# Kernel tuning notes

Hardware: AMD Instinct MI355X
Metric: run time of the kernel (lower is better)

Reference implementation:

```python
import jax, jax.numpy as jnp
import numpy as np

IN_F, OUT_F = 4096, 11008
B, S = 4, 512

def setup_inputs() -> dict:
    key = jax.random.key(0)
    k1, k2, k3, k4 = jax.random.split(key, 4)
    x = jax.random.normal(k1, (B, S, IN_F), dtype=jnp.float16)
    # int8 quantized weights in [-127, 127]
    weight_q = jax.random.randint(k2, (OUT_F, IN_F), -127, 128, dtype=jnp.int32).astype(jnp.int8)
    # per-output-channel scale, small positive values typical of int8 quant
    scale = (jax.random.uniform(k3, (OUT_F, 1), dtype=jnp.float32) * 0.02 + 0.001).astype(jnp.float16)
    bias = (jax.random.normal(k4, (OUT_F,), dtype=jnp.float32) * 0.02).astype(jnp.float16)
    return {"x": x, "weight_q": weight_q, "scale": scale, "bias": bias}

def reference(x, weight_q, scale, bias):
    # weight_deq = weight_q.to(fp16) * scale  -> [out, in] fp16 (materialized, as in torch)
    weight_deq = weight_q.astype(scale.dtype) * scale
    # F.linear: y = x @ W^T + b
    out = jnp.einsum('bsi,oi->bso', x, weight_deq) + bias
    return out
```

## Files before the change

kernel.cpp:

```cpp
#include <hip/hip_runtime.h>
#include <stdint.h>


#define M_DIM 2048
#define N_DIM 11008
#define K_DIM 4096
#define BM 128
#define BN 128
#define BK 32
#define NKT (K_DIM / BK)

#define NWQ (N_DIM * K_DIM / 4)
#define NXQ (M_DIM * K_DIM / 4)

typedef _Float16 f16x4 __attribute__((ext_vector_type(4)));
typedef _Float16 f16x8 __attribute__((ext_vector_type(8)));
typedef float    f32x4 __attribute__((ext_vector_type(4)));

__global__ __launch_bounds__(256)
void prep_w(const int* __restrict__ WQ, const float* __restrict__ SC,
            _Float16* __restrict__ W16)
{
  const int i = blockIdx.x * 256 + threadIdx.x;
  const int4 w = ((const int4*)WQ)[i];
  const float s = SC[i >> 10];
  f16x4 o = { (_Float16)(w.x * s), (_Float16)(w.y * s),
              (_Float16)(w.z * s), (_Float16)(w.w * s) };
  ((f16x4*)W16)[i] = o;
}

__global__ __launch_bounds__(256)
void prep_x(const float* __restrict__ X, _Float16* __restrict__ X16)
{
  const int i = blockIdx.x * 256 + threadIdx.x;
  const float4 v = ((const float4*)X)[i];
  f16x4 o = { (_Float16)v.x, (_Float16)v.y, (_Float16)v.z, (_Float16)v.w };
  ((f16x4*)X16)[i] = o;
}

__device__ __forceinline__ void async_cp16(void* lds, const void* g) {
  auto l = (__attribute__((address_space(3))) uint32_t*)(uintptr_t)lds;
  auto p = (const __attribute__((address_space(1))) uint32_t*)(uintptr_t)g;
  __builtin_amdgcn_global_load_lds(p, l, 16, 0, 0);
}

__global__ __launch_bounds__(256, 5)
void qlinear_gemm(const _Float16* __restrict__ A, const _Float16* __restrict__ B,
                  const float* __restrict__ BI, float* __restrict__ O)
{
  __shared__ __align__(16) _Float16 sA[2][BM * BK];
  __shared__ __align__(16) _Float16 sB[2][BN * BK];

  const int t    = threadIdx.x;
  const int lane = t & 63;
  const int wv   = t >> 6;
  const int wr   = wv >> 1;
  const int wc   = wv & 1;
  const int fr   = lane & 15;
  const int fq   = lane >> 4;

  const int wg = (blockIdx.x & 7) * 172 + (blockIdx.x >> 3);
  const int m0 = (wg & 15) * BM;
  const int n0 = (wg >> 4) * BN;

  const _Float16* gA0 = A + (size_t)(m0 + (t >> 2)) * K_DIM + (t & 3) * 8;
  const _Float16* gB0 = B + (size_t)(n0 + (t >> 2)) * K_DIM + (t & 3) * 8;
  const int wbase = t & 0xC0;
  _Float16* lA = &sA[0][0] + wbase * 8;
  _Float16* lB = &sB[0][0] + wbase * 8;

  f32x4 acc[4][4] = {};

#define STAGE(buf, kt) do {                                                    \
    const int ko_ = (kt) * BK;                                                 \
    async_cp16((void*)(lA + (buf) * (BM * BK)),        gA0 + ko_);             \
    async_cp16((void*)(lA + (buf) * (BM * BK) + 2048), gA0 + (size_t)64 * K_DIM + ko_); \
    async_cp16((void*)(lB + (buf) * (BN * BK)),        gB0 + ko_);             \
    async_cp16((void*)(lB + (buf) * (BN * BK) + 2048), gB0 + (size_t)64 * K_DIM + ko_); \
  } while (0)

  STAGE(0, 0);
  __syncthreads();

  for (int kt = 0; kt < NKT; ++kt) {
    const int cur = kt & 1;
    if (kt + 1 < NKT) STAGE(cur ^ 1, kt + 1);

    const _Float16* aB = &sA[cur][0] + (wr * 64 + fr) * BK + fq * 8;
    const _Float16* bB = &sB[cur][0] + (wc * 64 + fr) * BK + fq * 8;

    f16x8 af[4], bf[4];
#pragma unroll
    for (int i = 0; i < 4; ++i) af[i] = *(const f16x8*)(aB + i * 16 * BK);
#pragma unroll
    for (int i = 0; i < 4; ++i) bf[i] = *(const f16x8*)(bB + i * 16 * BK);

#pragma unroll
    for (int mi = 0; mi < 4; ++mi)
#pragma unroll
      for (int ni = 0; ni < 4; ++ni)
        acc[mi][ni] = __builtin_amdgcn_mfma_f32_16x16x32_f16(af[mi], bf[ni], acc[mi][ni], 0, 0, 0);

    __syncthreads();
  }

  const int om = m0 + wr * 64;
  const int on = n0 + wc * 64;
#pragma unroll
  for (int ni = 0; ni < 4; ++ni) {
    const int n = on + ni * 16 + fr;
    const float b = BI[n];
#pragma unroll
    for (int mi = 0; mi < 4; ++mi) {
      const int m = om + mi * 16 + fq * 4;
#pragma unroll
      for (int j = 0; j < 4; ++j) {
        const _Float16 h = (_Float16)acc[mi][ni][j];
        const _Float16 r = (_Float16)((float)h + b);
        O[(size_t)(m + j) * N_DIM + n] = (float)r;
      }
    }
  }
#undef STAGE
}

extern "C" void kernel_launch(void* const* d_in, const int* in_sizes, int n_in,
                              void* d_out, int out_size, void* d_ws, size_t ws_size,
                              hipStream_t stream) {
  const float* x  = (const float*)d_in[0];
  const int*   wq = (const int*)d_in[1];
  const float* sc = (const float*)d_in[2];
  const float* bi = (const float*)d_in[3];
  float* out = (float*)d_out;

  _Float16* x16 = (_Float16*)d_ws;
  _Float16* w16 = (_Float16*)((char*)d_ws + (size_t)M_DIM * K_DIM * 2);
  const size_t need = (size_t)M_DIM * K_DIM * 2 + (size_t)N_DIM * K_DIM * 2;
  if (ws_size < need) return;

  prep_w<<<dim3(NWQ / 256), dim3(256), 0, stream>>>(wq, sc, w16);
  prep_x<<<dim3(NXQ / 256), dim3(256), 0, stream>>>(x, x16);

  dim3 grid((M_DIM / BM) * (N_DIM / BN));
  qlinear_gemm<<<grid, dim3(256), 0, stream>>>(x16, w16, bi, out);
}
```

Before: 525.1 us.

## Fuse int8 weight dequantization into GEMM B-tile staging

Drops the separate prep_w pass, which read the int32-stored weights and wrote a full fp16 dequantized copy. The GEMM now loads int32 weight values straight into registers, multiplies by a per-row scale held in registers, and writes fp16 into LDS. The next tile's loads are issued before the MFMAs to overlap latency, and launch bounds drop from 5 to 3 blocks per SM. The cost is more VGPR pressure and conversion ALU work inside the main loop. Each weight is also re-read as 4-byte int32 by all 16 M-tiles instead of as 2-byte fp16, which doubles GEMM B-side traffic.

```diff
diff --git a/kernel.cpp b/kernel.cpp
--- a/kernel.cpp
+++ b/kernel.cpp
@@ -10,24 +10,11 @@
 #define BK 32
 #define NKT (K_DIM / BK)
 
-#define NWQ (N_DIM * K_DIM / 4)
 #define NXQ (M_DIM * K_DIM / 4)
 
 typedef _Float16 f16x4 __attribute__((ext_vector_type(4)));
 typedef _Float16 f16x8 __attribute__((ext_vector_type(8)));
 typedef float    f32x4 __attribute__((ext_vector_type(4)));
-
-__global__ __launch_bounds__(256)
-void prep_w(const int* __restrict__ WQ, const float* __restrict__ SC,
-            _Float16* __restrict__ W16)
-{
-  const int i = blockIdx.x * 256 + threadIdx.x;
-  const int4 w = ((const int4*)WQ)[i];
-  const float s = SC[i >> 10];
-  f16x4 o = { (_Float16)(w.x * s), (_Float16)(w.y * s),
-              (_Float16)(w.z * s), (_Float16)(w.w * s) };
-  ((f16x4*)W16)[i] = o;
-}
 
 __global__ __launch_bounds__(256)
 void prep_x(const float* __restrict__ X, _Float16* __restrict__ X16)
@@ -44,18 +31,19 @@
   __builtin_amdgcn_global_load_lds(p, l, 16, 0, 0);
 }
 
-__global__ __launch_bounds__(256, 5)
-void qlinear_gemm(const _Float16* __restrict__ A, const _Float16* __restrict__ B,
-                  const float* __restrict__ BI, float* __restrict__ O)
+__global__ __launch_bounds__(256, 3)
+void qlinear_gemm(const _Float16* __restrict__ A, const int* __restrict__ WQ,
+                  const float* __restrict__ SC, const float* __restrict__ BI,
+                  float* __restrict__ O)
 {
   __shared__ __align__(16) _Float16 sA[2][BM * BK];
   __shared__ __align__(16) _Float16 sB[2][BN * BK];
 
   const int t    = threadIdx.x;
   const int lane = t & 63;
-  const int wv   = t >> 6;
-  const int wr   = wv >> 1;
-  const int wc   = wv & 1;
+  const int wid  = t >> 6;
+  const int wr   = wid >> 1;
+  const int wc   = wid & 1;
   const int fr   = lane & 15;
   const int fq   = lane >> 4;
 
@@ -64,27 +52,51 @@
   const int n0 = (wg >> 4) * BN;
 
   const _Float16* gA0 = A + (size_t)(m0 + (t >> 2)) * K_DIM + (t & 3) * 8;
-  const _Float16* gB0 = B + (size_t)(n0 + (t >> 2)) * K_DIM + (t & 3) * 8;
   const int wbase = t & 0xC0;
   _Float16* lA = &sA[0][0] + wbase * 8;
-  _Float16* lB = &sB[0][0] + wbase * 8;
+
+  const int brow = t >> 3;
+  const int bkq  = t & 7;
+  const int* gB = WQ + (size_t)(n0 + brow) * K_DIM + bkq * 4;
+  float s[4];
+#pragma unroll
+  for (int r = 0; r < 4; ++r) s[r] = SC[n0 + 32 * r + brow];
+  _Float16* lBw = &sB[0][0] + brow * BK + bkq * 4;
 
   f32x4 acc[4][4] = {};
 
-#define STAGE(buf, kt) do {                                                    \
+#define STAGE_A(buf, kt) do {                                                  \
     const int ko_ = (kt) * BK;                                                 \
     async_cp16((void*)(lA + (buf) * (BM * BK)),        gA0 + ko_);             \
     async_cp16((void*)(lA + (buf) * (BM * BK) + 2048), gA0 + (size_t)64 * K_DIM + ko_); \
-    async_cp16((void*)(lB + (buf) * (BN * BK)),        gB0 + ko_);             \
-    async_cp16((void*)(lB + (buf) * (BN * BK) + 2048), gB0 + (size_t)64 * K_DIM + ko_); \
   } while (0)
 
-  STAGE(0, 0);
+  STAGE_A(0, 0);
+  {
+    int4 w0[4];
+#pragma unroll
+    for (int r = 0; r < 4; ++r)
+      w0[r] = *(const int4*)(gB + (size_t)32 * r * K_DIM);
+#pragma unroll
+    for (int r = 0; r < 4; ++r) {
+      f16x4 o = { (_Float16)(w0[r].x * s[r]), (_Float16)(w0[r].y * s[r]),
+                  (_Float16)(w0[r].z * s[r]), (_Float16)(w0[r].w * s[r]) };
+      *(f16x4*)(lBw + r * 32 * BK) = o;
+    }
+  }
   __syncthreads();
 
   for (int kt = 0; kt < NKT; ++kt) {
     const int cur = kt & 1;
-    if (kt + 1 < NKT) STAGE(cur ^ 1, kt + 1);
+    const bool pf = (kt + 1 < NKT);
+
+    int4 wnx[4];
+    if (pf) {
+      STAGE_A(cur ^ 1, kt + 1);
+#pragma unroll
+      for (int r = 0; r < 4; ++r)
+        wnx[r] = *(const int4*)(gB + (kt + 1) * BK + (size_t)32 * r * K_DIM);
+    }
 
     const _Float16* aB = &sA[cur][0] + (wr * 64 + fr) * BK + fq * 8;
     const _Float16* bB = &sB[cur][0] + (wc * 64 + fr) * BK + fq * 8;
@@ -101,6 +113,14 @@
       for (int ni = 0; ni < 4; ++ni)
         acc[mi][ni] = __builtin_amdgcn_mfma_f32_16x16x32_f16(af[mi], bf[ni], acc[mi][ni], 0, 0, 0);
 
+    if (pf) {
+#pragma unroll
+      for (int r = 0; r < 4; ++r) {
+        f16x4 o = { (_Float16)(wnx[r].x * s[r]), (_Float16)(wnx[r].y * s[r]),
+                    (_Float16)(wnx[r].z * s[r]), (_Float16)(wnx[r].w * s[r]) };
+        *(f16x4*)(lBw + (cur ^ 1) * (BM * BK) + r * 32 * BK) = o;
+      }
+    }
     __syncthreads();
   }
 
@@ -121,7 +141,7 @@
       }
     }
   }
-#undef STAGE
+#undef STAGE_A
 }
 
 extern "C" void kernel_launch(void* const* d_in, const int* in_sizes, int n_in,
@@ -134,13 +154,10 @@
   float* out = (float*)d_out;
 
   _Float16* x16 = (_Float16*)d_ws;
-  _Float16* w16 = (_Float16*)((char*)d_ws + (size_t)M_DIM * K_DIM * 2);
-  const size_t need = (size_t)M_DIM * K_DIM * 2 + (size_t)N_DIM * K_DIM * 2;
-  if (ws_size < need) return;
+  if (ws_size < (size_t)M_DIM * K_DIM * 2) return;
 
-  prep_w<<<dim3(NWQ / 256), dim3(256), 0, stream>>>(wq, sc, w16);
   prep_x<<<dim3(NXQ / 256), dim3(256), 0, stream>>>(x, x16);
 
   dim3 grid((M_DIM / BM) * (N_DIM / BN));
-  qlinear_gemm<<<grid, dim3(256), 0, stream>>>(x16, w16, bi, out);
+  qlinear_gemm<<<grid, dim3(256), 0, stream>>>(x16, wq, sc, bi, out);
 }
```

Result: slower. 572.9 us (+9.1%).

## Use 16-wave blocks with BK=64 and a triple-buffered async LDS pipeline

Applied to the files above, without the earlier changes.

The GEMM block grows from 4 to 16 waves. Each wave now owns a 32x32 sub-tile instead of 64x64, and the K tile doubles to 64. Shared memory becomes a three-slot ring with explicit vmcnt waits and raw barriers, so global-to-LDS copies run two stages ahead of compute. MFMA phases are split by s_setprio and extra barriers. The aim is better latency hiding and fewer loop iterations, at the cost of lower register reuse per wave (more LDS reads per MFMA), more barriers, and 96KB of LDS that limits occupancy.

```diff
diff --git a/kernel.cpp b/kernel.cpp
--- a/kernel.cpp
+++ b/kernel.cpp
@@ -7,7 +7,7 @@
 #define K_DIM 4096
 #define BM 128
 #define BN 128
-#define BK 32
+#define BK 64
 #define NKT (K_DIM / BK)
 
 #define NWQ (N_DIM * K_DIM / 4)
@@ -44,18 +44,18 @@
   __builtin_amdgcn_global_load_lds(p, l, 16, 0, 0);
 }
 
-__global__ __launch_bounds__(256, 5)
+__global__ __launch_bounds__(1024, 4)
 void qlinear_gemm(const _Float16* __restrict__ A, const _Float16* __restrict__ B,
                   const float* __restrict__ BI, float* __restrict__ O)
 {
-  __shared__ __align__(16) _Float16 sA[2][BM * BK];
-  __shared__ __align__(16) _Float16 sB[2][BN * BK];
+  __shared__ __align__(16) _Float16 sA[3][BM * BK];
+  __shared__ __align__(16) _Float16 sB[3][BN * BK];
 
   const int t    = threadIdx.x;
   const int lane = t & 63;
-  const int wv   = t >> 6;
-  const int wr   = wv >> 1;
-  const int wc   = wv & 1;
+  const int wid  = t >> 6;
+  const int wr   = wid >> 2;
+  const int wc   = wid & 3;
   const int fr   = lane & 15;
   const int fq   = lane >> 4;
 
@@ -63,59 +63,85 @@
   const int m0 = (wg & 15) * BM;
   const int n0 = (wg >> 4) * BN;
 
-  const _Float16* gA0 = A + (size_t)(m0 + (t >> 2)) * K_DIM + (t & 3) * 8;
-  const _Float16* gB0 = B + (size_t)(n0 + (t >> 2)) * K_DIM + (t & 3) * 8;
-  const int wbase = t & 0xC0;
-  _Float16* lA = &sA[0][0] + wbase * 8;
-  _Float16* lB = &sB[0][0] + wbase * 8;
+  const _Float16* gA0 = A + (size_t)(m0 + (t >> 3)) * K_DIM + (t & 7) * 8;
+  const _Float16* gB0 = B + (size_t)(n0 + (t >> 3)) * K_DIM + (t & 7) * 8;
+  const int wchunk = t & ~63;
+  _Float16* lA = &sA[0][0] + wchunk * 8;
+  _Float16* lB = &sB[0][0] + wchunk * 8;
 
-  f32x4 acc[4][4] = {};
+  f32x4 acc[2][2] = {};
 
-#define STAGE(buf, kt) do {                                                    \
-    const int ko_ = (kt) * BK;                                                 \
-    async_cp16((void*)(lA + (buf) * (BM * BK)),        gA0 + ko_);             \
-    async_cp16((void*)(lA + (buf) * (BM * BK) + 2048), gA0 + (size_t)64 * K_DIM + ko_); \
-    async_cp16((void*)(lB + (buf) * (BN * BK)),        gB0 + ko_);             \
-    async_cp16((void*)(lB + (buf) * (BN * BK) + 2048), gB0 + (size_t)64 * K_DIM + ko_); \
+#define STAGE(slot, kt) do {                                       \
+    async_cp16((void*)(lA + (slot) * (BM * BK)), gA0 + (kt) * BK); \
+    async_cp16((void*)(lB + (slot) * (BN * BK)), gB0 + (kt) * BK); \
   } while (0)
 
   STAGE(0, 0);
-  __syncthreads();
+  STAGE(1, 1);
 
+  int s = 0;
   for (int kt = 0; kt < NKT; ++kt) {
-    const int cur = kt & 1;
-    if (kt + 1 < NKT) STAGE(cur ^ 1, kt + 1);
+    const int s2 = (s + 2 >= 3) ? s - 1 : s + 2;
 
-    const _Float16* aB = &sA[cur][0] + (wr * 64 + fr) * BK + fq * 8;
-    const _Float16* bB = &sB[cur][0] + (wc * 64 + fr) * BK + fq * 8;
+    if (kt < NKT - 1) asm volatile("s_waitcnt vmcnt(2)" ::: "memory");
+    else              asm volatile("s_waitcnt vmcnt(0)" ::: "memory");
+    __builtin_amdgcn_s_barrier();
+    __builtin_amdgcn_sched_barrier(0);
 
-    f16x8 af[4], bf[4];
+    const _Float16* aP = &sA[s][0] + (wr * 32 + fr) * BK + fq * 8;
+    const _Float16* bP = &sB[s][0] + (wc * 32 + fr) * BK + fq * 8;
+
+    if (kt + 2 < NKT) STAGE(s2, kt + 2);
+
+    f16x8 bf[2][2], af0[2];
 #pragma unroll
-    for (int i = 0; i < 4; ++i) af[i] = *(const f16x8*)(aB + i * 16 * BK);
+    for (int nf = 0; nf < 2; ++nf)
 #pragma unroll
-    for (int i = 0; i < 4; ++i) bf[i] = *(const f16x8*)(bB + i * 16 * BK);
+      for (int kk = 0; kk < 2; ++kk)
+        bf[nf][kk] = *(const f16x8*)(bP + nf * 16 * BK + kk * 32);
+#pragma unroll
+    for (int kk = 0; kk < 2; ++kk)
+      af0[kk] = *(const f16x8*)(aP + kk * 32);
 
+    __builtin_amdgcn_s_setprio(1);
 #pragma unroll
-    for (int mi = 0; mi < 4; ++mi)
+    for (int kk = 0; kk < 2; ++kk)
 #pragma unroll
-      for (int ni = 0; ni < 4; ++ni)
-        acc[mi][ni] = __builtin_amdgcn_mfma_f32_16x16x32_f16(af[mi], bf[ni], acc[mi][ni], 0, 0, 0);
+      for (int nf = 0; nf < 2; ++nf)
+        acc[0][nf] = __builtin_amdgcn_mfma_f32_16x16x32_f16(af0[kk], bf[nf][kk], acc[0][nf], 0, 0, 0);
+    __builtin_amdgcn_s_setprio(0);
 
-    __syncthreads();
+    __builtin_amdgcn_s_barrier();
+    __builtin_amdgcn_sched_barrier(0);
+
+    f16x8 af1[2];
+#pragma unroll
+    for (int kk = 0; kk < 2; ++kk)
+      af1[kk] = *(const f16x8*)(aP + 16 * BK + kk * 32);
+
+    __builtin_amdgcn_s_setprio(1);
+#pragma unroll
+    for (int kk = 0; kk < 2; ++kk)
+#pragma unroll
+      for (int nf = 0; nf < 2; ++nf)
+        acc[1][nf] = __builtin_amdgcn_mfma_f32_16x16x32_f16(af1[kk], bf[nf][kk], acc[1][nf], 0, 0, 0);
+    __builtin_amdgcn_s_setprio(0);
+
+    s = (s + 1 == 3) ? 0 : s + 1;
   }
 
-  const int om = m0 + wr * 64;
-  const int on = n0 + wc * 64;
+  const int om = m0 + wr * 32;
+  const int on = n0 + wc * 32;
 #pragma unroll
-  for (int ni = 0; ni < 4; ++ni) {
-    const int n = on + ni * 16 + fr;
+  for (int nf = 0; nf < 2; ++nf) {
+    const int n = on + nf * 16 + fr;
     const float b = BI[n];
 #pragma unroll
-    for (int mi = 0; mi < 4; ++mi) {
-      const int m = om + mi * 16 + fq * 4;
+    for (int mf = 0; mf < 2; ++mf) {
+      const int m = om + mf * 16 + fq * 4;
 #pragma unroll
       for (int j = 0; j < 4; ++j) {
-        const _Float16 h = (_Float16)acc[mi][ni][j];
+        const _Float16 h = (_Float16)acc[mf][nf][j];
         const _Float16 r = (_Float16)((float)h + b);
         O[(size_t)(m + j) * N_DIM + n] = (float)r;
       }
@@ -142,5 +168,5 @@
   prep_x<<<dim3(NXQ / 256), dim3(256), 0, stream>>>(x, x16);
 
   dim3 grid((M_DIM / BM) * (N_DIM / BN));
-  qlinear_gemm<<<grid, dim3(256), 0, stream>>>(x16, w16, bi, out);
+  qlinear_gemm<<<grid, dim3(1024), 0, stream>>>(x16, w16, bi, out);
 }
```

New measurement: 718.8 us. 1.37x slower.
